# Performance work log

Hardware: AMD Instinct MI355X
Metric: run time of the kernel (lower is better)

## Reference

```python
import jax, jax.numpy as jnp
import numpy as np

T = 256          # n_tokens
APR = 3          # atoms_per_residue
N = T * APR      # n_atoms = 768
CA = 128         # atom_embedding_size
CP = 16          # atom_pair_embedding_size
CT = 384         # token_embedding_size
CS = 384         # single_embedding_size
CZ = 128         # pair_embedding_size
NB = 3           # num_block
H = 4            # num_head
DH = CA // H
NQ = 32          # num_queries (query block size)
NK = 128         # num_keys (local key window)


def _ln(x, g, b):
    m = jnp.mean(x, -1, keepdims=True)
    v = jnp.mean((x - m) ** 2, -1, keepdims=True)
    return (x - m) * jax.lax.rsqrt(v + 1e-5) * g + b


def setup_inputs() -> dict:
    key = jax.random.key(0)
    ks = jax.random.split(key, 32)
    w = lambda k, shape: jax.random.normal(k, shape, jnp.float32) * 0.02
    return {
        "ref_pos": jax.random.normal(ks[0], (N, 3), jnp.float32),
        "ref_space_uid": jax.random.randint(ks[1], (N,), 0, T),
        "r": jax.random.normal(ks[2], (N, 3), jnp.float32),
        "s": jax.random.normal(ks[3], (T, CS), jnp.float32),
        "z": jax.random.normal(ks[4], (T, T, CZ), jnp.float32),
        "W_pos": w(ks[5], (3, CA)),
        "W_pos_offset": w(ks[6], (3, CP)),
        "W_inv_sq_dist": w(ks[7], (1, CP)),
        "W_mask": w(ks[8], (1, CP)),
        "W_cond_a": w(ks[9], (CA, CP)),
        "W_cond_b": w(ks[10], (CA, CP)),
        "ln_s_g": jnp.ones((CS,), jnp.float32), "ln_s_b": jnp.zeros((CS,), jnp.float32),
        "W_single": w(ks[11], (CS, CA)),
        "ln_z_g": jnp.ones((CZ,), jnp.float32), "ln_z_b": jnp.zeros((CZ,), jnp.float32),
        "W_pair": w(ks[12], (CZ, CP)),
        "W_noisy": w(ks[13], (3, CA)),
        "W_mlp1": w(ks[14], (CP, CP)),
        "W_mlp2": w(ks[15], (CP, CP)),
        "W_mlp3": w(ks[16], (CP, CP)),
        "at_ln_g": jnp.ones((NB, CA), jnp.float32), "at_ln_b": jnp.zeros((NB, CA), jnp.float32),
        "at_Wq": w(ks[17], (NB, CA, CA)),
        "at_Wk": w(ks[18], (NB, CA, CA)),
        "at_Wv": w(ks[19], (NB, CA, CA)),
        "at_Wg": w(ks[20], (NB, CA, CA)),
        "at_lnp_g": jnp.ones((NB, CP), jnp.float32), "at_lnp_b": jnp.zeros((NB, CP), jnp.float32),
        "at_Wb": w(ks[21], (NB, CP, H)),
        "at_Wo": w(ks[22], (NB, CA, CA)),
        "at_ln2_g": jnp.ones((NB, CA), jnp.float32), "at_ln2_b": jnp.zeros((NB, CA), jnp.float32),
        "at_Wt1": w(ks[23], (NB, CA, 4 * CA)),
        "at_Wt2": w(ks[24], (NB, 4 * CA, CA)),
        "W_proj": w(ks[25], (CA, CT)),
    }


def _forward(ref_pos, ref_space_uid, r, s, z, W_pos, W_pos_offset, W_inv_sq_dist, W_mask,
             W_cond_a, W_cond_b, ln_s_g, ln_s_b, W_single, ln_z_g, ln_z_b, W_pair, W_noisy,
             W_mlp1, W_mlp2, W_mlp3, at_ln_g, at_ln_b, at_Wq, at_Wk, at_Wv, at_Wg,
             at_lnp_g, at_lnp_b, at_Wb, at_Wo, at_ln2_g, at_ln2_b, at_Wt1, at_Wt2, W_proj):
    c = ref_pos @ W_pos                                             # [N,CA]
    dist = ref_pos[:, None, :] - ref_pos[None, :, :]                # [N,N,3]
    maskf = (ref_space_uid[:, None] == ref_space_uid[None, :])[..., None].astype(jnp.float32)
    pair = (dist @ W_pos_offset) * maskf                            # [N,N,CP]
    sq = jnp.sum(dist * dist, -1, keepdims=True)                    # [N,N,1]
    pair = pair + ((1.0 / (1.0 + sq)) @ W_inv_sq_dist) * maskf
    pair = pair + (maskf @ W_mask) * maskf
    q = c
    # r is not None branch
    c = c + _ln(jnp.tile(s, (APR, 1)), ln_s_g, ln_s_b) @ W_single
    pair = pair + _ln(jnp.tile(z, (APR, APR, 1)), ln_z_g, ln_z_b) @ W_pair
    q = q + r @ W_noisy
    rc = jax.nn.relu(c)
    pair = pair + (rc @ W_cond_a)[:, None, :] + (rc @ W_cond_b)[None, :, :]
    h = jax.nn.relu(pair) @ W_mlp1
    h = jax.nn.relu(h) @ W_mlp2
    h = jax.nn.relu(h) @ W_mlp3
    pair = pair + h
    # sequence-local attention mask (AF3-style: query blocks of NQ attend a NK-wide window)
    idx = jnp.arange(N)
    center = (idx // NQ) * NQ + (NQ - 1) / 2.0
    beta = jnp.where(jnp.abs(idx[None, :].astype(jnp.float32) - center[:, None]) < NK / 2.0, 0.0, -1e9)
    scale = 1.0 / np.sqrt(DH).astype(np.float32)
    x = q
    for b in range(NB):
        a = _ln(x, at_ln_g[b], at_ln_b[b])
        qh = (a @ at_Wq[b]).reshape(N, H, DH)
        kh = (a @ at_Wk[b]).reshape(N, H, DH)
        vh = (a @ at_Wv[b]).reshape(N, H, DH)
        bias = _ln(pair, at_lnp_g[b], at_lnp_b[b]) @ at_Wb[b]       # [N,N,H]
        logits = jnp.einsum('ihd,jhd->hij', qh, kh) * scale + bias.transpose(2, 0, 1) + beta[None]
        attn = jax.nn.softmax(logits, axis=-1)
        o = jnp.einsum('hij,jhd->ihd', attn, vh)
        g = jax.nn.sigmoid(a @ at_Wg[b]).reshape(N, H, DH)
        x = x + (o * g).reshape(N, CA) @ at_Wo[b]
        t = _ln(x, at_ln2_g[b], at_ln2_b[b])
        x = x + jax.nn.relu(t @ at_Wt1[b]) @ at_Wt2[b]
    qout = jax.nn.relu(x @ W_proj)                                  # [N,CT]
    a_out = jnp.mean(qout.reshape(T, APR, CT), axis=-2)             # [T,CT]
    return a_out, qout, c, pair


def reference(ref_pos, ref_space_uid, r, s, z, W_pos, W_pos_offset, W_inv_sq_dist, W_mask,
              W_cond_a, W_cond_b, ln_s_g, ln_s_b, W_single, ln_z_g, ln_z_b, W_pair, W_noisy,
              W_mlp1, W_mlp2, W_mlp3, at_ln_g, at_ln_b, at_Wq, at_Wk, at_Wv, at_Wg,
              at_lnp_g, at_lnp_b, at_Wb, at_Wo, at_ln2_g, at_ln2_b, at_Wt1, at_Wt2, W_proj):
    return _forward(ref_pos, ref_space_uid, r, s, z, W_pos, W_pos_offset, W_inv_sq_dist, W_mask,
                    W_cond_a, W_cond_b, ln_s_g, ln_s_b, W_single, ln_z_g, ln_z_b, W_pair, W_noisy,
                    W_mlp1, W_mlp2, W_mlp3, at_ln_g, at_ln_b, at_Wq, at_Wk, at_Wv, at_Wg,
                    at_lnp_g, at_lnp_b, at_Wb, at_Wo, at_ln2_g, at_ln2_b, at_Wt1, at_Wt2, W_proj)
```

## Files before the change

### kernel.cpp

```cpp
#include <hip/hip_runtime.h>
#include <math.h>


__device__ __forceinline__ float sigmoidf_(float v) { return 1.f / (1.f + __expf(-v)); }

typedef __attribute__((ext_vector_type(4))) short s16x4;
typedef __attribute__((ext_vector_type(8))) short s16x8;
typedef __attribute__((ext_vector_type(4))) float f32x4;

__device__ __forceinline__ unsigned bfpack(float a, float b) {
  return (__float_as_uint(a) >> 16) | (__float_as_uint(b) & 0xFFFF0000u);
}
__device__ __forceinline__ short bf1(float a) { return (short)(__float_as_uint(a) >> 16); }

__global__ __launch_bounds__(128) void k_tokatoms(
    const float* __restrict__ s, const float* __restrict__ g,
    const float* __restrict__ b, const float* __restrict__ W_single,
    const float* __restrict__ ref_pos, const float* __restrict__ r,
    const float* __restrict__ W_pos, const float* __restrict__ W_noisy,
    const float* __restrict__ Wca, const float* __restrict__ Wcb,
    float* __restrict__ c_out, float* __restrict__ x,
    float* __restrict__ ca, float* __restrict__ cb) {
  int tok = blockIdx.x, t = threadIdx.x;
  __shared__ float sln[384];
  __shared__ float ws[48 * 128];
  __shared__ float red[4];
  __shared__ float rc[128];
  float v0 = s[tok * 384 + t], v1 = s[tok * 384 + 128 + t], v2 = s[tok * 384 + 256 + t];
  float ps = v0 + v1 + v2, pq = v0 * v0 + v1 * v1 + v2 * v2;
#pragma unroll
  for (int o = 1; o < 64; o <<= 1) { ps += __shfl_xor(ps, o); pq += __shfl_xor(pq, o); }
  if ((t & 63) == 0) { red[t >> 6] = ps; red[2 + (t >> 6)] = pq; }
  __syncthreads();
  float mean = (red[0] + red[1]) * (1.f / 384.f);
  float var = (red[2] + red[3]) * (1.f / 384.f) - mean * mean;
  float rstd = rsqrtf(var + 1e-5f);
  sln[t] = (v0 - mean) * rstd * g[t] + b[t];
  sln[128 + t] = (v1 - mean) * rstd * g[128 + t] + b[128 + t];
  sln[256 + t] = (v2 - mean) * rstd * g[256 + t] + b[256 + t];
  float ctv = 0.f;
  for (int c0 = 0; c0 < 384; c0 += 48) {
    __syncthreads();
#pragma unroll
    for (int m = 0; m < 12; m++) {
      int idx = (t + 128 * m) * 4;
      *(float4*)&ws[idx] = *(const float4*)&W_single[c0 * 128 + idx];
    }
    __syncthreads();
#pragma unroll 8
    for (int kk = 0; kk < 48; kk++) ctv += sln[c0 + kk] * ws[kk * 128 + t];
  }
  float wp0 = W_pos[t], wp1 = W_pos[128 + t], wp2 = W_pos[256 + t];
  float wn0 = W_noisy[t], wn1 = W_noisy[128 + t], wn2 = W_noisy[256 + t];
#pragma unroll
  for (int a = 0; a < 3; a++) {
    int i = tok + 256 * a;
    float p0 = ref_pos[i * 3], p1 = ref_pos[i * 3 + 1], p2 = ref_pos[i * 3 + 2];
    float r0 = r[i * 3], r1 = r[i * 3 + 1], r2 = r[i * 3 + 2];
    float c0 = p0 * wp0 + p1 * wp1 + p2 * wp2;
    x[i * 128 + t] = c0 + r0 * wn0 + r1 * wn1 + r2 * wn2;
    float cc = c0 + ctv;
    c_out[i * 128 + t] = cc;
    __syncthreads();
    rc[t] = fmaxf(cc, 0.f);
    __syncthreads();
    int out_id = t >> 2, q = t & 3;
    const float* Wm = (out_id < 16) ? Wca : Wcb;
    int ch = out_id & 15;
    float acc = 0.f;
#pragma unroll
    for (int kk = 0; kk < 32; kk++) { int k = q * 32 + kk; acc += rc[k] * Wm[k * 16 + ch]; }
    acc += __shfl_xor(acc, 1);
    acc += __shfl_xor(acc, 2);
    if (q == 0) { if (out_id < 16) ca[i * 16 + ch] = acc; else cb[i * 16 + ch] = acc; }
  }
}

__global__ __launch_bounds__(256) void k_zp(
    const float* __restrict__ z, const float* __restrict__ g,
    const float* __restrict__ lb, const float* __restrict__ W_pair,
    float* __restrict__ zp) {
  __shared__ float wT[16][132];
  __shared__ float zs[16][132];
  __shared__ float sWg[16], Bc[16];
  int t = threadIdx.x;
#pragma unroll
  for (int m = 0; m < 8; m++) {
    int e = t + 256 * m;
    int row = e >> 4, ch = e & 15;
    wT[ch][row] = g[row] * W_pair[e];
  }
  __syncthreads();
  if (t < 32) {
    int ch = t & 15;
    float a = 0.f;
    if (t < 16) {
#pragma unroll 8
      for (int k = 0; k < 128; k++) a += wT[ch][k];
      sWg[ch] = a;
    } else {
#pragma unroll 8
      for (int k = 0; k < 128; k++) a += lb[k] * W_pair[k * 16 + ch];
      Bc[ch] = a;
    }
  }
  int row = t >> 4, kk = (t & 15) * 8;
  long base = ((long)blockIdx.x * 16 + row) * 128 + kk;
  float4 a4 = *(const float4*)&z[base];
  float4 b4 = *(const float4*)&z[base + 4];
  *(float4*)&zs[row][kk] = a4;
  *(float4*)&zs[row][kk + 4] = b4;
  float ps = a4.x + a4.y + a4.z + a4.w + b4.x + b4.y + b4.z + b4.w;
  float pq = a4.x * a4.x + a4.y * a4.y + a4.z * a4.z + a4.w * a4.w +
             b4.x * b4.x + b4.y * b4.y + b4.z * b4.z + b4.w * b4.w;
#pragma unroll
  for (int o = 1; o < 16; o <<= 1) { ps += __shfl_xor(ps, o); pq += __shfl_xor(pq, o); }
  float m = ps * (1.f / 128.f);
  float rstd = rsqrtf(pq * (1.f / 128.f) - m * m + 1e-5f);
  __syncthreads();
  int ch = t & 15;
  float dotv = 0.f;
#pragma unroll 8
  for (int k4 = 0; k4 < 32; k4++) {
    float4 zv = *(float4*)&zs[row][k4 * 4];
    float4 wv = *(float4*)&wT[ch][k4 * 4];
    dotv += zv.x * wv.x + zv.y * wv.y + zv.z * wv.z + zv.w * wv.w;
  }
  zp[((long)blockIdx.x * 16 + row) * 16 + ch] = rstd * (dotv - m * sWg[ch]) + Bc[ch];
}

__global__ __launch_bounds__(256) void k_pairM(
    const float* __restrict__ ref_pos, const int* __restrict__ uid,
    const float* __restrict__ Wpo, const float* __restrict__ Wisd,
    const float* __restrict__ Wmask, const float* __restrict__ W1,
    const float* __restrict__ W2, const float* __restrict__ W3,
    const float* __restrict__ zp, const float* __restrict__ ca,
    const float* __restrict__ cb, const float* __restrict__ lnp_g,
    const float* __restrict__ lnp_b, const float* __restrict__ Wb,
    float* __restrict__ pair_out, float* __restrict__ biasA) {
  int i = blockIdx.x / 3, jb = blockIdx.x % 3, t = threadIdx.x;
  __shared__ float jsx[256], jsy[256], jsz[256];
  __shared__ int jsu[256];
  __shared__ __align__(128) short stg[4][1280];
  __shared__ __align__(16) float pfs[4][1056];
  __shared__ float wgb[192];
  __shared__ float kbs[12];
  int jg = jb * 256 + t;
  jsx[t] = ref_pos[jg * 3];
  jsy[t] = ref_pos[jg * 3 + 1];
  jsz[t] = ref_pos[jg * 3 + 2];
  jsu[t] = uid[jg];
  if (t >= 64) {
    int e = t - 64;
    if (e < 192) {
      int bq = e >> 6, k = (e >> 2) & 15, h = e & 3;
      wgb[e] = lnp_g[bq * 16 + k] * Wb[bq * 64 + k * 4 + h];
    }
  }
  if (t >= 48 && t < 60) {
    int e = t - 48, bq = e >> 2, h = e & 3;
    float a = 0.f;
#pragma unroll
    for (int cc = 0; cc < 16; cc++) a += lnp_b[bq * 16 + cc] * Wb[bq * 64 + cc * 4 + h];
    kbs[e] = a;
  }
  int w = t >> 6, l = t & 63;
  int c = l & 15, gr = l >> 4;
  float pix = ref_pos[i * 3], piy = ref_pos[i * 3 + 1], piz = ref_pos[i * 3 + 2];
  int ui = uid[i];
  float w0c = Wpo[c], w1c = Wpo[16 + c], w2c = Wpo[32 + c];
  float wic = Wisd[c], wmc = Wmask[c], cac = ca[i * 16 + c];
  s16x8 bw0 = {bf1(W1[(4 * gr + 0) * 16 + c]), bf1(W1[(4 * gr + 1) * 16 + c]),
               bf1(W1[(4 * gr + 2) * 16 + c]), bf1(W1[(4 * gr + 3) * 16 + c]),
               (short)0, (short)0, (short)0, (short)0};
  s16x8 bw1 = {bf1(W2[(4 * gr + 0) * 16 + c]), bf1(W2[(4 * gr + 1) * 16 + c]),
               bf1(W2[(4 * gr + 2) * 16 + c]), bf1(W2[(4 * gr + 3) * 16 + c]),
               (short)0, (short)0, (short)0, (short)0};
  s16x8 bw2 = {bf1(W3[(4 * gr + 0) * 16 + c]), bf1(W3[(4 * gr + 1) * 16 + c]),
               bf1(W3[(4 * gr + 2) * 16 + c]), bf1(W3[(4 * gr + 3) * 16 + c]),
               (short)0, (short)0, (short)0, (short)0};
  __syncthreads();
  char* sb = (char*)&stg[w][0];
  unsigned sbase = (unsigned)(uintptr_t)sb;
  f32x4 z4 = {0.f, 0.f, 0.f, 0.f};
#pragma unroll
  for (int g = 0; g < 4; g++) {
    float p0_, p1_, p2_, p3_;
    {
      int jl0 = w * 64 + g * 16 + 4 * gr;
#pragma unroll
      for (int r = 0; r < 4; r++) {
        int jloc = jl0 + r;
        int j = jb * 256 + jloc;
        float d0 = pix - jsx[jloc], d1 = piy - jsy[jloc], d2 = piz - jsz[jloc];
        float mk = (ui == jsu[jloc]) ? 1.f : 0.f;
        float inv = 1.f / (1.f + d0 * d0 + d1 * d1 + d2 * d2);
        float zv = zp[((long)((i & 255) << 8) + jloc) * 16 + c];
        float cbv = cb[j * 16 + c];
        float pv = mk * (d0 * w0c + d1 * w1c + d2 * w2c + inv * wic + wmc) + zv + cbv + cac;
        if (r == 0) p0_ = pv; else if (r == 1) p1_ = pv; else if (r == 2) p2_ = pv; else p3_ = pv;
      }
    }
    char* wp = sb + g * 640 + c * 32 + gr * 8;
    unsigned ra = sbase + (unsigned)(g * 640 + c * 8 + gr * 128);
    *(uint2*)wp = make_uint2(bfpack(fmaxf(p0_, 0.f), fmaxf(p1_, 0.f)),
                             bfpack(fmaxf(p2_, 0.f), fmaxf(p3_, 0.f)));
    s16x4 tr0;
    asm volatile("s_waitcnt lgkmcnt(0)\n\tds_read_b64_tr_b16 %0, %1\n\ts_waitcnt lgkmcnt(0)"
                 : "=v"(tr0) : "v"(ra) : "memory");
    s16x8 a8 = {tr0[0], tr0[1], tr0[2], tr0[3], (short)0, (short)0, (short)0, (short)0};
    f32x4 h1 = __builtin_amdgcn_mfma_f32_16x16x32_bf16(a8, bw0, z4, 0, 0, 0);
    *(uint2*)wp = make_uint2(bfpack(fmaxf(h1[0], 0.f), fmaxf(h1[1], 0.f)),
                             bfpack(fmaxf(h1[2], 0.f), fmaxf(h1[3], 0.f)));
    s16x4 tr1;
    asm volatile("s_waitcnt lgkmcnt(0)\n\tds_read_b64_tr_b16 %0, %1\n\ts_waitcnt lgkmcnt(0)"
                 : "=v"(tr1) : "v"(ra) : "memory");
    s16x8 a8b = {tr1[0], tr1[1], tr1[2], tr1[3], (short)0, (short)0, (short)0, (short)0};
    f32x4 h2 = __builtin_amdgcn_mfma_f32_16x16x32_bf16(a8b, bw1, z4, 0, 0, 0);
    *(uint2*)wp = make_uint2(bfpack(fmaxf(h2[0], 0.f), fmaxf(h2[1], 0.f)),
                             bfpack(fmaxf(h2[2], 0.f), fmaxf(h2[3], 0.f)));
    s16x4 tr2;
    asm volatile("s_waitcnt lgkmcnt(0)\n\tds_read_b64_tr_b16 %0, %1\n\ts_waitcnt lgkmcnt(0)"
                 : "=v"(tr2) : "v"(ra) : "memory");
    s16x8 a8c = {tr2[0], tr2[1], tr2[2], tr2[3], (short)0, (short)0, (short)0, (short)0};
    f32x4 h3 = __builtin_amdgcn_mfma_f32_16x16x32_bf16(a8c, bw2, z4, 0, 0, 0);
    float f0 = p0_ + h3[0], f1 = p1_ + h3[1], f2 = p2_ + h3[2], f3 = p3_ + h3[3];
    {
      int jl0 = w * 64 + g * 16 + 4 * gr;
      long pb = ((long)i * 768 + (long)(jb * 256 + jl0)) * 16 + c;
      pair_out[pb] = f0;
      pair_out[pb + 16] = f1;
      pair_out[pb + 32] = f2;
      pair_out[pb + 48] = f3;
    }
    *(float4*)&pfs[w][g * 264 + c * 16 + 4 * gr] = make_float4(f0, f1, f2, f3);
  }
  asm volatile("s_waitcnt lgkmcnt(0)" ::: "memory");
  int qb = i >> 5;
  int j = jb * 256 + t;
  unsigned jw = (unsigned)(j - (qb * 32 - 48));
  if (jw < 128u) {
    int gt = (t >> 4) & 3, jr = t & 15;
    float v[16];
#pragma unroll
    for (int cc = 0; cc < 16; cc++) v[cc] = pfs[w][gt * 264 + cc * 16 + jr];
    float m = 0.f;
#pragma unroll
    for (int cc = 0; cc < 16; cc++) m += v[cc];
    m *= (1.f / 16.f);
    float vv = 0.f;
#pragma unroll
    for (int cc = 0; cc < 16; cc++) { float d = v[cc] - m; vv += d * d; }
    float rs = rsqrtf(vv * (1.f / 16.f) + 1e-5f);
    float nrm[16];
#pragma unroll
    for (int cc = 0; cc < 16; cc++) nrm[cc] = (v[cc] - m) * rs;
    int qi = i & 31;
#pragma unroll
    for (int bq = 0; bq < 3; bq++) {
      float o0 = kbs[bq * 4 + 0], o1 = kbs[bq * 4 + 1];
      float o2 = kbs[bq * 4 + 2], o3 = kbs[bq * 4 + 3];
#pragma unroll
      for (int k = 0; k < 16; k++) {
        float nv = nrm[k];
        float4 wv = *(float4*)&wgb[bq * 64 + k * 4];
        o0 += nv * wv.x; o1 += nv * wv.y; o2 += nv * wv.z; o3 += nv * wv.w;
      }
      long base = (long)(bq * 96 + qb * 4) * 4096 + (long)qi * 128 + jw;
      biasA[base] = o0;
      biasA[base + 4096] = o1;
      biasA[base + 2 * 4096] = o2;
      biasA[base + 3 * 4096] = o3;
    }
  }
}

__global__ __launch_bounds__(256) void k_qkvg(
    const float* __restrict__ x, const float* __restrict__ lng,
    const float* __restrict__ lnb, const float* __restrict__ Wq,
    const float* __restrict__ Wk, const float* __restrict__ Wv,
    const float* __restrict__ Wg, float* __restrict__ qkvg) {
  __shared__ float As[128][18];
  __shared__ float Ws[128][66];
  int t = threadIdx.x;
  int rb = blockIdx.x >> 3, bn = blockIdx.x & 7;
  int r0 = rb * 16;
  const float* Wm = (bn < 2) ? Wq : (bn < 4) ? Wk : (bn < 6) ? Wv : Wg;
  int c0 = (bn & 1) * 64;
  int ncol0 = (bn >> 1) * 128 + c0;
#pragma unroll
  for (int m = 0; m < 8; m++) {
    int idx = t + 256 * m;
    int row = idx >> 4, c4 = (idx & 15) * 4;
    *(float4*)&Ws[row][c4] = *(const float4*)&Wm[row * 128 + c0 + c4];
  }
  {
    int rr = t >> 4, tt = t & 15;
    int row = r0 + rr;
    float4 x0 = *(const float4*)&x[row * 128 + tt * 8];
    float4 x1 = *(const float4*)&x[row * 128 + tt * 8 + 4];
    float ps = x0.x + x0.y + x0.z + x0.w + x1.x + x1.y + x1.z + x1.w;
    float pq = x0.x * x0.x + x0.y * x0.y + x0.z * x0.z + x0.w * x0.w +
               x1.x * x1.x + x1.y * x1.y + x1.z * x1.z + x1.w * x1.w;
#pragma unroll
    for (int o = 1; o < 16; o <<= 1) { ps += __shfl_xor(ps, o); pq += __shfl_xor(pq, o); }
    float m = ps * (1.f / 128.f);
    float rstd = rsqrtf(pq * (1.f / 128.f) - m * m + 1e-5f);
    float4 g0 = *(const float4*)&lng[tt * 8], g1 = *(const float4*)&lng[tt * 8 + 4];
    float4 b0 = *(const float4*)&lnb[tt * 8], b1 = *(const float4*)&lnb[tt * 8 + 4];
    As[tt * 8 + 0][rr] = (x0.x - m) * rstd * g0.x + b0.x;
    As[tt * 8 + 1][rr] = (x0.y - m) * rstd * g0.y + b0.y;
    As[tt * 8 + 2][rr] = (x0.z - m) * rstd * g0.z + b0.z;
    As[tt * 8 + 3][rr] = (x0.w - m) * rstd * g0.w + b0.w;
    As[tt * 8 + 4][rr] = (x1.x - m) * rstd * g1.x + b1.x;
    As[tt * 8 + 5][rr] = (x1.y - m) * rstd * g1.y + b1.y;
    As[tt * 8 + 6][rr] = (x1.z - m) * rstd * g1.z + b1.z;
    As[tt * 8 + 7][rr] = (x1.w - m) * rstd * g1.w + b1.w;
  }
  __syncthreads();
  int ty = t >> 5, tx = t & 31;
  float a00 = 0, a01 = 0, a10 = 0, a11 = 0;
#pragma unroll 8
  for (int k = 0; k < 128; k++) {
    float2 a2 = *(float2*)&As[k][ty * 2];
    float2 w2 = *(float2*)&Ws[k][tx * 2];
    a00 += a2.x * w2.x; a01 += a2.x * w2.y;
    a10 += a2.y * w2.x; a11 += a2.y * w2.y;
  }
  int row = r0 + ty * 2;
  float2 o0 = {a00, a01}, o1 = {a10, a11};
  *(float2*)&qkvg[row * 512 + ncol0 + tx * 2] = o0;
  *(float2*)&qkvg[(row + 1) * 512 + ncol0 + tx * 2] = o1;
}

__global__ __launch_bounds__(256) void k_attn2(
    const float* __restrict__ qkvg, const float* __restrict__ biasb,
    float* __restrict__ og) {
  int qt = blockIdx.x >> 2, h = blockIdx.x & 3, t = threadIdx.x;
  int i0 = qt * 16;
  int qb32 = qt >> 1;
  int lo = qb32 * 32 - 48;
  int qoff = (qt & 1) * 16;
  __shared__ float qs[16][36];
  __shared__ float ks[128][36];
  __shared__ float vs[128][36];
  __shared__ float L[16][132];
  {
    int e = t * 8;
    int qi = e >> 7, k8 = e & 127;
    const float* bb = &biasb[(long)(qb32 * 4 + h) * 4096 + (long)(qoff + qi) * 128];
#pragma unroll
    for (int m = 0; m < 2; m++) {
      int k4 = k8 + m * 4;
      int j4 = lo + k4;
      float4 bv;
      if (j4 >= 0 && j4 <= 764) bv = *(const float4*)&bb[k4];
      else bv = make_float4(-1e30f, -1e30f, -1e30f, -1e30f);
      *(float4*)&L[qi][k4] = bv;
    }
  }
  if (t < 128) {
    int qi = t >> 3, dq = (t & 7) * 4;
    *(float4*)&qs[qi][dq] = *(const float4*)&qkvg[(i0 + qi) * 512 + h * 32 + dq];
  }
  {
    int kj = t >> 1, dh = (t & 1) * 16;
    int j = lo + kj;
    if (j >= 0 && j < 768) {
      const float4* sk = (const float4*)&qkvg[j * 512 + 128 + h * 32 + dh];
      const float4* sv = (const float4*)&qkvg[j * 512 + 256 + h * 32 + dh];
#pragma unroll
      for (int m = 0; m < 4; m++) {
        *(float4*)&ks[kj][dh + 4 * m] = sk[m];
        *(float4*)&vs[kj][dh + 4 * m] = sv[m];
      }
    } else {
      float4 zz = {0, 0, 0, 0};
#pragma unroll
      for (int m = 0; m < 4; m++) {
        *(float4*)&ks[kj][dh + 4 * m] = zz;
        *(float4*)&vs[kj][dh + 4 * m] = zz;
      }
    }
  }
  __syncthreads();
  const float scale = 0.17677669529663687f;
  {
    int qi = t & 15, kb = t >> 4;
    float4 qr[8];
#pragma unroll
    for (int m = 0; m < 8; m++) qr[m] = *(float4*)&qs[qi][m * 4];
#pragma unroll
    for (int kk = 0; kk < 8; kk++) {
      int kj = kb * 8 + kk;
      float acc = 0.f;
#pragma unroll
      for (int m = 0; m < 8; m++) {
        float4 kv = *(float4*)&ks[kj][m * 4];
        acc += qr[m].x * kv.x + qr[m].y * kv.y + qr[m].z * kv.z + qr[m].w * kv.w;
      }
      L[qi][kj] += acc * scale;
    }
  }
  __syncthreads();
  int qi = t >> 4, sg = t & 15;
  float mx = -1e30f;
#pragma unroll
  for (int k2 = 0; k2 < 8; k2++) mx = fmaxf(mx, L[qi][sg * 8 + k2]);
#pragma unroll
  for (int o = 1; o < 16; o <<= 1) mx = fmaxf(mx, __shfl_xor(mx, o));
  float sum = 0.f;
#pragma unroll
  for (int k2 = 0; k2 < 8; k2++) {
    int kj = sg * 8 + k2;
    float e = __expf(L[qi][kj] - mx);
    L[qi][kj] = e;
    sum += e;
  }
#pragma unroll
  for (int o = 1; o < 16; o <<= 1) sum += __shfl_xor(sum, o);
  float rden = 1.f / sum;
  __syncthreads();
  {
    int d2 = (t & 15) * 2;
    float a0 = 0.f, a1 = 0.f;
#pragma unroll 8
    for (int kj = 0; kj < 128; kj++) {
      float p = L[qi][kj];
      float2 v = *(float2*)&vs[kj][d2];
      a0 += p * v.x; a1 += p * v.y;
    }
    int i = i0 + qi;
    float2 gr = *(const float2*)&qkvg[i * 512 + 384 + h * 32 + d2];
    float2 o2;
    o2.x = a0 * rden * sigmoidf_(gr.x);
    o2.y = a1 * rden * sigmoidf_(gr.y);
    *(float2*)&og[i * 128 + h * 32 + d2] = o2;
  }
}

template <int MODE>
__global__ __launch_bounds__(384) void k_fusedT(
    const float* __restrict__ og, const float* __restrict__ Wo,
    const float* __restrict__ g2, const float* __restrict__ b2,
    const float* __restrict__ Wt1, const float* __restrict__ Wt2,
    float* __restrict__ x,
    const float* __restrict__ lng_n, const float* __restrict__ lnb_n,
    const float* __restrict__ Wq, const float* __restrict__ Wk,
    const float* __restrict__ Wv, const float* __restrict__ Wg,
    float* __restrict__ qkvg, const float* __restrict__ W_proj,
    float* __restrict__ out) {
  int t = threadIdx.x;
  int r0 = blockIdx.x * 3;
  __shared__ float osr[3][128];
  __shared__ float xns[3][128];
  __shared__ float asr[3][128];
  __shared__ float hs[3][512];
  __shared__ float part[4][3][128];
  __shared__ float red[12];
  {
    int rr = t >> 7, c = t & 127;
    osr[rr][c] = og[(r0 + rr) * 128 + c];
    xns[rr][c] = x[(r0 + rr) * 128 + c];
  }
  __syncthreads();
  {
    int c4 = (t & 31) * 4, row = (t >> 5) % 3, q = t / 96;
    int k0 = q * 32;
    float a0 = 0.f, a1 = 0.f, a2 = 0.f, a3 = 0.f;
#pragma unroll 8
    for (int kk = 0; kk < 32; kk++) {
      int k = k0 + kk;
      float4 w = *(const float4*)&Wo[k * 128 + c4];
      float av = osr[row][k];
      a0 += av * w.x; a1 += av * w.y; a2 += av * w.z; a3 += av * w.w;
    }
    *(float4*)&part[q][row][c4] = make_float4(a0, a1, a2, a3);
  }
  __syncthreads();
  {
    int rr = t >> 7, c = t & 127;
    float xv = xns[rr][c] + part[0][rr][c] + part[1][rr][c] + part[2][rr][c] + part[3][rr][c];
    float ps = xv, pq = xv * xv;
#pragma unroll
    for (int o = 1; o < 64; o <<= 1) { ps += __shfl_xor(ps, o); pq += __shfl_xor(pq, o); }
    int wv = t >> 6;
    if ((t & 63) == 0) { red[wv] = ps; red[6 + wv] = pq; }
    __syncthreads();
    float mean = (red[2 * rr] + red[2 * rr + 1]) * (1.f / 128.f);
    float var = (red[6 + 2 * rr] + red[6 + 2 * rr + 1]) * (1.f / 128.f) - mean * mean;
    float rstd = rsqrtf(var + 1e-5f);
    xns[rr][c] = xv;
    asr[rr][c] = (xv - mean) * rstd * g2[c] + b2[c];
  }
  __syncthreads();
  {
    int c4 = (t & 127) * 4, row = t >> 7;
    float a0 = 0.f, a1 = 0.f, a2 = 0.f, a3 = 0.f;
#pragma unroll 8
    for (int k = 0; k < 128; k++) {
      float4 w = *(const float4*)&Wt1[k * 512 + c4];
      float av = asr[row][k];
      a0 += av * w.x; a1 += av * w.y; a2 += av * w.z; a3 += av * w.w;
    }
    *(float4*)&hs[row][c4] = make_float4(fmaxf(a0, 0.f), fmaxf(a1, 0.f),
                                         fmaxf(a2, 0.f), fmaxf(a3, 0.f));
  }
  __syncthreads();
  {
    int c4 = (t & 31) * 4, row = (t >> 5) % 3, q = t / 96;
    int k0 = q * 128;
    float a0 = 0.f, a1 = 0.f, a2 = 0.f, a3 = 0.f;
#pragma unroll 8
    for (int kk = 0; kk < 128; kk++) {
      int k = k0 + kk;
      float4 w = *(const float4*)&Wt2[k * 128 + c4];
      float hv = hs[row][k];
      a0 += hv * w.x; a1 += hv * w.y; a2 += hv * w.z; a3 += hv * w.w;
    }
    *(float4*)&part[q][row][c4] = make_float4(a0, a1, a2, a3);
  }
  __syncthreads();
  {
    int rr = t >> 7, c = t & 127;
    float xf = xns[rr][c] + part[0][rr][c] + part[1][rr][c] +
               part[2][rr][c] + part[3][rr][c];
    x[(r0 + rr) * 128 + c] = xf;
    xns[rr][c] = xf;
  }
  if (MODE == 1) {
    __syncthreads();
    {
      int rr = t >> 7, c = t & 127;
      float xv = xns[rr][c];
      float ps = xv, pq = xv * xv;
#pragma unroll
      for (int o = 1; o < 64; o <<= 1) { ps += __shfl_xor(ps, o); pq += __shfl_xor(pq, o); }
      int wv = t >> 6;
      if ((t & 63) == 0) { red[wv] = ps; red[6 + wv] = pq; }
      __syncthreads();
      float mean = (red[2 * rr] + red[2 * rr + 1]) * (1.f / 128.f);
      float var = (red[6 + 2 * rr] + red[6 + 2 * rr + 1]) * (1.f / 128.f) - mean * mean;
      float rstd = rsqrtf(var + 1e-5f);
      asr[rr][c] = (xv - mean) * rstd * lng_n[c] + lnb_n[c];
    }
    __syncthreads();
    {
      int c4 = (t & 127) * 4, row = t >> 7;
      int mtx = c4 >> 7, lc = c4 & 127;
      const float* Wm = (mtx == 0) ? Wq : (mtx == 1) ? Wk : (mtx == 2) ? Wv : Wg;
      float a0 = 0.f, a1 = 0.f, a2 = 0.f, a3 = 0.f;
#pragma unroll 8
      for (int k = 0; k < 128; k++) {
        float4 w = *(const float4*)&Wm[k * 128 + lc];
        float av = asr[row][k];
        a0 += av * w.x; a1 += av * w.y; a2 += av * w.z; a3 += av * w.w;
      }
      *(float4*)&qkvg[(r0 + row) * 512 + c4] = make_float4(a0, a1, a2, a3);
    }
  }
  if (MODE == 2) {
    __syncthreads();
    int tk = blockIdx.x;
    float a0 = 0.f, a1 = 0.f, a2 = 0.f;
#pragma unroll 8
    for (int k = 0; k < 128; k++) {
      float w = W_proj[k * 384 + t];
      a0 += xns[0][k] * w; a1 += xns[1][k] * w; a2 += xns[2][k] * w;
    }
    a0 = fmaxf(a0, 0.f); a1 = fmaxf(a1, 0.f); a2 = fmaxf(a2, 0.f);
    out[98304 + (tk * 3 + 0) * 384 + t] = a0;
    out[98304 + (tk * 3 + 1) * 384 + t] = a1;
    out[98304 + (tk * 3 + 2) * 384 + t] = a2;
    out[tk * 384 + t] = (a0 + a1 + a2) * (1.f / 3.f);
  }
}

extern "C" void kernel_launch(void* const* d_in, const int* in_sizes, int n_in,
                              void* d_out, int out_size, void* d_ws, size_t ws_size,
                              hipStream_t stream) {
  const float* ref_pos  = (const float*)d_in[0];
  const int*   uid      = (const int*)d_in[1];
  const float* r        = (const float*)d_in[2];
  const float* s        = (const float*)d_in[3];
  const float* z        = (const float*)d_in[4];
  const float* W_pos    = (const float*)d_in[5];
  const float* Wpo      = (const float*)d_in[6];
  const float* Wisd     = (const float*)d_in[7];
  const float* Wmask    = (const float*)d_in[8];
  const float* Wca      = (const float*)d_in[9];
  const float* Wcb      = (const float*)d_in[10];
  const float* ln_s_g   = (const float*)d_in[11];
  const float* ln_s_b   = (const float*)d_in[12];
  const float* W_single = (const float*)d_in[13];
  const float* ln_z_g   = (const float*)d_in[14];
  const float* ln_z_b   = (const float*)d_in[15];
  const float* W_pair   = (const float*)d_in[16];
  const float* W_noisy  = (const float*)d_in[17];
  const float* W_mlp1   = (const float*)d_in[18];
  const float* W_mlp2   = (const float*)d_in[19];
  const float* W_mlp3   = (const float*)d_in[20];
  const float* at_ln_g  = (const float*)d_in[21];
  const float* at_ln_b  = (const float*)d_in[22];
  const float* at_Wq    = (const float*)d_in[23];
  const float* at_Wk    = (const float*)d_in[24];
  const float* at_Wv    = (const float*)d_in[25];
  const float* at_Wg    = (const float*)d_in[26];
  const float* at_lnp_g = (const float*)d_in[27];
  const float* at_lnp_b = (const float*)d_in[28];
  const float* at_Wb    = (const float*)d_in[29];
  const float* at_Wo    = (const float*)d_in[30];
  const float* at_ln2_g = (const float*)d_in[31];
  const float* at_ln2_b = (const float*)d_in[32];
  const float* at_Wt1   = (const float*)d_in[33];
  const float* at_Wt2   = (const float*)d_in[34];
  const float* W_proj   = (const float*)d_in[35];
  float* out = (float*)d_out;
  float* W = (float*)d_ws;
  float* x     = W;
  float* ca    = W + 98304;
  float* cb    = W + 110592;
  float* zp    = W + 122880;
  float* biasA = W + 1171456;
  float* qkvg  = W + 2351104;
  float* og    = W + 2744320;

  k_zp<<<4096, 256, 0, stream>>>(z, ln_z_g, ln_z_b, W_pair, zp);
  k_tokatoms<<<256, 128, 0, stream>>>(s, ln_s_g, ln_s_b, W_single, ref_pos, r,
                                      W_pos, W_noisy, Wca, Wcb,
                                      out + 393216, x, ca, cb);
  k_pairM<<<2304, 256, 0, stream>>>(ref_pos, uid, Wpo, Wisd, Wmask, W_mlp1, W_mlp2,
                                    W_mlp3, zp, ca, cb, at_lnp_g, at_lnp_b, at_Wb,
                                    out + 491520, biasA);
  k_qkvg<<<384, 256, 0, stream>>>(x, at_ln_g, at_ln_b, at_Wq, at_Wk, at_Wv, at_Wg, qkvg);
  k_attn2<<<192, 256, 0, stream>>>(qkvg, biasA, og);
  k_fusedT<1><<<256, 384, 0, stream>>>(og, at_Wo, at_ln2_g, at_ln2_b, at_Wt1, at_Wt2, x,
                                       at_ln_g + 128, at_ln_b + 128,
                                       at_Wq + 16384, at_Wk + 16384,
                                       at_Wv + 16384, at_Wg + 16384, qkvg,
                                       nullptr, nullptr);
  k_attn2<<<192, 256, 0, stream>>>(qkvg, biasA + 393216, og);
  k_fusedT<1><<<256, 384, 0, stream>>>(og, at_Wo + 16384, at_ln2_g + 128, at_ln2_b + 128,
                                       at_Wt1 + 65536, at_Wt2 + 65536, x,
                                       at_ln_g + 256, at_ln_b + 256,
                                       at_Wq + 32768, at_Wk + 32768,
                                       at_Wv + 32768, at_Wg + 32768, qkvg,
                                       nullptr, nullptr);
  k_attn2<<<192, 256, 0, stream>>>(qkvg, biasA + 786432, og);
  k_fusedT<2><<<256, 384, 0, stream>>>(og, at_Wo + 32768, at_ln2_g + 256, at_ln2_b + 256,
                                       at_Wt1 + 131072, at_Wt2 + 131072, x,
                                       nullptr, nullptr, nullptr, nullptr,
                                       nullptr, nullptr, nullptr, W_proj, out);
}
```

Measured before the change: 158.4 us.

## Merge independent front-end kernels into shared launches to cut launch count

```diff
diff --git a/kernel.cpp b/kernel.cpp
--- a/kernel.cpp
+++ b/kernel.cpp
@@ -13,7 +13,10 @@
 }
 __device__ __forceinline__ short bf1(float a) { return (short)(__float_as_uint(a) >> 16); }
 
-__global__ __launch_bounds__(128) void k_tokatoms(
+__global__ __launch_bounds__(256) void k_front(
+    const float* __restrict__ z, const float* __restrict__ zg,
+    const float* __restrict__ zlb, const float* __restrict__ W_pair,
+    float* __restrict__ zp,
     const float* __restrict__ s, const float* __restrict__ g,
     const float* __restrict__ b, const float* __restrict__ W_single,
     const float* __restrict__ ref_pos, const float* __restrict__ r,
@@ -21,115 +24,130 @@
     const float* __restrict__ Wca, const float* __restrict__ Wcb,
     float* __restrict__ c_out, float* __restrict__ x,
     float* __restrict__ ca, float* __restrict__ cb) {
-  int tok = blockIdx.x, t = threadIdx.x;
-  __shared__ float sln[384];
-  __shared__ float ws[48 * 128];
-  __shared__ float red[4];
-  __shared__ float rc[128];
-  float v0 = s[tok * 384 + t], v1 = s[tok * 384 + 128 + t], v2 = s[tok * 384 + 256 + t];
-  float ps = v0 + v1 + v2, pq = v0 * v0 + v1 * v1 + v2 * v2;
-#pragma unroll
-  for (int o = 1; o < 64; o <<= 1) { ps += __shfl_xor(ps, o); pq += __shfl_xor(pq, o); }
-  if ((t & 63) == 0) { red[t >> 6] = ps; red[2 + (t >> 6)] = pq; }
-  __syncthreads();
-  float mean = (red[0] + red[1]) * (1.f / 384.f);
-  float var = (red[2] + red[3]) * (1.f / 384.f) - mean * mean;
-  float rstd = rsqrtf(var + 1e-5f);
-  sln[t] = (v0 - mean) * rstd * g[t] + b[t];
-  sln[128 + t] = (v1 - mean) * rstd * g[128 + t] + b[128 + t];
-  sln[256 + t] = (v2 - mean) * rstd * g[256 + t] + b[256 + t];
-  float ctv = 0.f;
-  for (int c0 = 0; c0 < 384; c0 += 48) {
-    __syncthreads();
-#pragma unroll
-    for (int m = 0; m < 12; m++) {
-      int idx = (t + 128 * m) * 4;
-      *(float4*)&ws[idx] = *(const float4*)&W_single[c0 * 128 + idx];
-    }
-    __syncthreads();
-#pragma unroll 8
-    for (int kk = 0; kk < 48; kk++) ctv += sln[c0 + kk] * ws[kk * 128 + t];
-  }
-  float wp0 = W_pos[t], wp1 = W_pos[128 + t], wp2 = W_pos[256 + t];
-  float wn0 = W_noisy[t], wn1 = W_noisy[128 + t], wn2 = W_noisy[256 + t];
-#pragma unroll
-  for (int a = 0; a < 3; a++) {
-    int i = tok + 256 * a;
-    float p0 = ref_pos[i * 3], p1 = ref_pos[i * 3 + 1], p2 = ref_pos[i * 3 + 2];
-    float r0 = r[i * 3], r1 = r[i * 3 + 1], r2 = r[i * 3 + 2];
-    float c0 = p0 * wp0 + p1 * wp1 + p2 * wp2;
-    x[i * 128 + t] = c0 + r0 * wn0 + r1 * wn1 + r2 * wn2;
-    float cc = c0 + ctv;
-    c_out[i * 128 + t] = cc;
-    __syncthreads();
-    rc[t] = fmaxf(cc, 0.f);
-    __syncthreads();
-    int out_id = t >> 2, q = t & 3;
-    const float* Wm = (out_id < 16) ? Wca : Wcb;
-    int ch = out_id & 15;
-    float acc = 0.f;
-#pragma unroll
-    for (int kk = 0; kk < 32; kk++) { int k = q * 32 + kk; acc += rc[k] * Wm[k * 16 + ch]; }
-    acc += __shfl_xor(acc, 1);
-    acc += __shfl_xor(acc, 2);
-    if (q == 0) { if (out_id < 16) ca[i * 16 + ch] = acc; else cb[i * 16 + ch] = acc; }
+  __shared__ __align__(16) float sm[4624];
+  int t = threadIdx.x;
+  int bid = blockIdx.x;
+  if (bid < 4096) {
+    float* wT = sm;
+    float* zs = sm + 2112;
+    float* sWg = sm + 4224;
+    float* Bc = sm + 4240;
+#pragma unroll
+    for (int m = 0; m < 8; m++) {
+      int e = t + 256 * m;
+      int row = e >> 4, ch = e & 15;
+      wT[ch * 132 + row] = zg[row] * W_pair[e];
+    }
+    __syncthreads();
+    if (t < 32) {
+      int ch = t & 15;
+      float a = 0.f;
+      if (t < 16) {
+#pragma unroll 8
+        for (int k = 0; k < 128; k++) a += wT[ch * 132 + k];
+        sWg[ch] = a;
+      } else {
+#pragma unroll 8
+        for (int k = 0; k < 128; k++) a += zlb[k] * W_pair[k * 16 + ch];
+        Bc[ch] = a;
+      }
+    }
+    int row = t >> 4, kk = (t & 15) * 8;
+    long base = ((long)bid * 16 + row) * 128 + kk;
+    float4 a4 = *(const float4*)&z[base];
+    float4 b4 = *(const float4*)&z[base + 4];
+    *(float4*)&zs[row * 132 + kk] = a4;
+    *(float4*)&zs[row * 132 + kk + 4] = b4;
+    float ps = a4.x + a4.y + a4.z + a4.w + b4.x + b4.y + b4.z + b4.w;
+    float pq = a4.x * a4.x + a4.y * a4.y + a4.z * a4.z + a4.w * a4.w +
+               b4.x * b4.x + b4.y * b4.y + b4.z * b4.z + b4.w * b4.w;
+#pragma unroll
+    for (int o = 1; o < 16; o <<= 1) { ps += __shfl_xor(ps, o); pq += __shfl_xor(pq, o); }
+    float m = ps * (1.f / 128.f);
+    float rstd = rsqrtf(pq * (1.f / 128.f) - m * m + 1e-5f);
+    __syncthreads();
+    int ch = t & 15;
+    float dotv = 0.f;
+#pragma unroll 8
+    for (int k4 = 0; k4 < 32; k4++) {
+      float4 zv = *(float4*)&zs[row * 132 + k4 * 4];
+      float4 wv = *(float4*)&wT[ch * 132 + k4 * 4];
+      dotv += zv.x * wv.x + zv.y * wv.y + zv.z * wv.z + zv.w * wv.w;
+    }
+    zp[((long)bid * 16 + row) * 16 + ch] = rstd * (dotv - m * sWg[ch]) + Bc[ch];
+  } else {
+    int tok = bid - 4096;
+    float* sln = sm;
+    float* ws = sm + 384;
+    float* red = sm + 4480;
+    float* rc = sm + 4488;
+    float v0 = 0.f, v1 = 0.f, v2 = 0.f;
+    if (t < 128) {
+      v0 = s[tok * 384 + t]; v1 = s[tok * 384 + 128 + t]; v2 = s[tok * 384 + 256 + t];
+      float ps = v0 + v1 + v2, pq = v0 * v0 + v1 * v1 + v2 * v2;
+#pragma unroll
+      for (int o = 1; o < 64; o <<= 1) { ps += __shfl_xor(ps, o); pq += __shfl_xor(pq, o); }
+      if ((t & 63) == 0) { red[t >> 6] = ps; red[2 + (t >> 6)] = pq; }
+    }
+    __syncthreads();
+    float ctv = 0.f;
+    if (t < 128) {
+      float mean = (red[0] + red[1]) * (1.f / 384.f);
+      float var = (red[2] + red[3]) * (1.f / 384.f) - mean * mean;
+      float rstd = rsqrtf(var + 1e-5f);
+      sln[t] = (v0 - mean) * rstd * g[t] + b[t];
+      sln[128 + t] = (v1 - mean) * rstd * g[128 + t] + b[128 + t];
+      sln[256 + t] = (v2 - mean) * rstd * g[256 + t] + b[256 + t];
+    }
+    for (int c0 = 0; c0 < 384; c0 += 32) {
+      __syncthreads();
+#pragma unroll
+      for (int m = 0; m < 4; m++) {
+        int idx = (t + 256 * m) * 4;
+        *(float4*)&ws[idx] = *(const float4*)&W_single[c0 * 128 + idx];
+      }
+      __syncthreads();
+      if (t < 128) {
+#pragma unroll 8
+        for (int kk = 0; kk < 32; kk++) ctv += sln[c0 + kk] * ws[kk * 128 + t];
+      }
+    }
+    float wp0 = 0.f, wp1 = 0.f, wp2 = 0.f, wn0 = 0.f, wn1 = 0.f, wn2 = 0.f;
+    if (t < 128) {
+      wp0 = W_pos[t]; wp1 = W_pos[128 + t]; wp2 = W_pos[256 + t];
+      wn0 = W_noisy[t]; wn1 = W_noisy[128 + t]; wn2 = W_noisy[256 + t];
+    }
+#pragma unroll
+    for (int a = 0; a < 3; a++) {
+      int i = tok + 256 * a;
+      float cc = 0.f;
+      if (t < 128) {
+        float p0 = ref_pos[i * 3], p1 = ref_pos[i * 3 + 1], p2 = ref_pos[i * 3 + 2];
+        float r0 = r[i * 3], r1 = r[i * 3 + 1], r2 = r[i * 3 + 2];
+        float c0 = p0 * wp0 + p1 * wp1 + p2 * wp2;
+        x[i * 128 + t] = c0 + r0 * wn0 + r1 * wn1 + r2 * wn2;
+        cc = c0 + ctv;
+        c_out[i * 128 + t] = cc;
+      }
+      __syncthreads();
+      if (t < 128) rc[t] = fmaxf(cc, 0.f);
+      __syncthreads();
+      if (t < 128) {
+        int out_id = t >> 2, q = t & 3;
+        const float* Wm = (out_id < 16) ? Wca : Wcb;
+        int ch = out_id & 15;
+        float acc = 0.f;
+#pragma unroll
+        for (int kk = 0; kk < 32; kk++) { int k = q * 32 + kk; acc += rc[k] * Wm[k * 16 + ch]; }
+        acc += __shfl_xor(acc, 1);
+        acc += __shfl_xor(acc, 2);
+        if (q == 0) { if (out_id < 16) ca[i * 16 + ch] = acc; else cb[i * 16 + ch] = acc; }
+      }
+    }
   }
 }
 
-__global__ __launch_bounds__(256) void k_zp(
-    const float* __restrict__ z, const float* __restrict__ g,
-    const float* __restrict__ lb, const float* __restrict__ W_pair,
-    float* __restrict__ zp) {
-  __shared__ float wT[16][132];
-  __shared__ float zs[16][132];
-  __shared__ float sWg[16], Bc[16];
-  int t = threadIdx.x;
-#pragma unroll
-  for (int m = 0; m < 8; m++) {
-    int e = t + 256 * m;
-    int row = e >> 4, ch = e & 15;
-    wT[ch][row] = g[row] * W_pair[e];
-  }
-  __syncthreads();
-  if (t < 32) {
-    int ch = t & 15;
-    float a = 0.f;
-    if (t < 16) {
-#pragma unroll 8
-      for (int k = 0; k < 128; k++) a += wT[ch][k];
-      sWg[ch] = a;
-    } else {
-#pragma unroll 8
-      for (int k = 0; k < 128; k++) a += lb[k] * W_pair[k * 16 + ch];
-      Bc[ch] = a;
-    }
-  }
-  int row = t >> 4, kk = (t & 15) * 8;
-  long base = ((long)blockIdx.x * 16 + row) * 128 + kk;
-  float4 a4 = *(const float4*)&z[base];
-  float4 b4 = *(const float4*)&z[base + 4];
-  *(float4*)&zs[row][kk] = a4;
-  *(float4*)&zs[row][kk + 4] = b4;
-  float ps = a4.x + a4.y + a4.z + a4.w + b4.x + b4.y + b4.z + b4.w;
-  float pq = a4.x * a4.x + a4.y * a4.y + a4.z * a4.z + a4.w * a4.w +
-             b4.x * b4.x + b4.y * b4.y + b4.z * b4.z + b4.w * b4.w;
-#pragma unroll
-  for (int o = 1; o < 16; o <<= 1) { ps += __shfl_xor(ps, o); pq += __shfl_xor(pq, o); }
-  float m = ps * (1.f / 128.f);
-  float rstd = rsqrtf(pq * (1.f / 128.f) - m * m + 1e-5f);
-  __syncthreads();
-  int ch = t & 15;
-  float dotv = 0.f;
-#pragma unroll 8
-  for (int k4 = 0; k4 < 32; k4++) {
-    float4 zv = *(float4*)&zs[row][k4 * 4];
-    float4 wv = *(float4*)&wT[ch][k4 * 4];
-    dotv += zv.x * wv.x + zv.y * wv.y + zv.z * wv.z + zv.w * wv.w;
-  }
-  zp[((long)blockIdx.x * 16 + row) * 16 + ch] = rstd * (dotv - m * sWg[ch]) + Bc[ch];
-}
-
-__global__ __launch_bounds__(256) void k_pairM(
+__global__ __launch_bounds__(256) void k_pairq(
     const float* __restrict__ ref_pos, const int* __restrict__ uid,
     const float* __restrict__ Wpo, const float* __restrict__ Wisd,
     const float* __restrict__ Wmask, const float* __restrict__ W1,
@@ -137,14 +155,54 @@
     const float* __restrict__ zp, const float* __restrict__ ca,
     const float* __restrict__ cb, const float* __restrict__ lnp_g,
     const float* __restrict__ lnp_b, const float* __restrict__ Wb,
-    float* __restrict__ pair_out, float* __restrict__ biasA) {
-  int i = blockIdx.x / 3, jb = blockIdx.x % 3, t = threadIdx.x;
+    float* __restrict__ pair_out, float* __restrict__ biasA,
+    const float* __restrict__ x, const float* __restrict__ lng,
+    const float* __restrict__ lnb, const float* __restrict__ Wq,
+    const float* __restrict__ Wk, const float* __restrict__ Wv,
+    const float* __restrict__ Wg, float* __restrict__ qkvg) {
   __shared__ float jsx[256], jsy[256], jsz[256];
   __shared__ int jsu[256];
   __shared__ __align__(128) short stg[4][1280];
   __shared__ __align__(16) float pfs[4][1056];
   __shared__ float wgb[192];
   __shared__ float kbs[12];
+  int t = threadIdx.x;
+  int bid = blockIdx.x;
+  if (bid >= 2304) {
+    int r0 = (bid - 2304) * 2;
+    float* asr_ = jsx;
+    float* red_ = jsy;
+    int row = t >> 7, c = t & 127;
+    float xv = x[(r0 + row) * 128 + c];
+    {
+      float ps = xv, pq = xv * xv;
+#pragma unroll
+      for (int o = 1; o < 64; o <<= 1) { ps += __shfl_xor(ps, o); pq += __shfl_xor(pq, o); }
+      int wv = t >> 6;
+      if ((t & 63) == 0) { red_[wv] = ps; red_[4 + wv] = pq; }
+      __syncthreads();
+      float mean = (red_[2 * row] + red_[2 * row + 1]) * (1.f / 128.f);
+      float var = (red_[4 + 2 * row] + red_[4 + 2 * row + 1]) * (1.f / 128.f) - mean * mean;
+      float rstd = rsqrtf(var + 1e-5f);
+      asr_[row * 128 + c] = (xv - mean) * rstd * lng[c] + lnb[c];
+    }
+    __syncthreads();
+    {
+      int c4 = (t & 127) * 4, row2 = t >> 7;
+      int mtx = c4 >> 7, lc = c4 & 127;
+      const float* Wm = (mtx == 0) ? Wq : (mtx == 1) ? Wk : (mtx == 2) ? Wv : Wg;
+      float a0 = 0.f, a1 = 0.f, a2 = 0.f, a3 = 0.f;
+#pragma unroll 8
+      for (int k = 0; k < 128; k++) {
+        float4 w = *(const float4*)&Wm[k * 128 + lc];
+        float av = asr_[row2 * 128 + k];
+        a0 += av * w.x; a1 += av * w.y; a2 += av * w.z; a3 += av * w.w;
+      }
+      *(float4*)&qkvg[(r0 + row2) * 512 + c4] = make_float4(a0, a1, a2, a3);
+    }
+    return;
+  }
+  int i = bid / 3, jb = bid % 3;
   int jg = jb * 256 + t;
   jsx[t] = ref_pos[jg * 3];
   jsy[t] = ref_pos[jg * 3 + 1];
@@ -273,64 +331,6 @@
       biasA[base + 3 * 4096] = o3;
     }
   }
-}
-
-__global__ __launch_bounds__(256) void k_qkvg(
-    const float* __restrict__ x, const float* __restrict__ lng,
-    const float* __restrict__ lnb, const float* __restrict__ Wq,
-    const float* __restrict__ Wk, const float* __restrict__ Wv,
-    const float* __restrict__ Wg, float* __restrict__ qkvg) {
-  __shared__ float As[128][18];
-  __shared__ float Ws[128][66];
-  int t = threadIdx.x;
-  int rb = blockIdx.x >> 3, bn = blockIdx.x & 7;
-  int r0 = rb * 16;
-  const float* Wm = (bn < 2) ? Wq : (bn < 4) ? Wk : (bn < 6) ? Wv : Wg;
-  int c0 = (bn & 1) * 64;
-  int ncol0 = (bn >> 1) * 128 + c0;
-#pragma unroll
-  for (int m = 0; m < 8; m++) {
-    int idx = t + 256 * m;
-    int row = idx >> 4, c4 = (idx & 15) * 4;
-    *(float4*)&Ws[row][c4] = *(const float4*)&Wm[row * 128 + c0 + c4];
-  }
-  {
-    int rr = t >> 4, tt = t & 15;
-    int row = r0 + rr;
-    float4 x0 = *(const float4*)&x[row * 128 + tt * 8];
-    float4 x1 = *(const float4*)&x[row * 128 + tt * 8 + 4];
-    float ps = x0.x + x0.y + x0.z + x0.w + x1.x + x1.y + x1.z + x1.w;
-    float pq = x0.x * x0.x + x0.y * x0.y + x0.z * x0.z + x0.w * x0.w +
-               x1.x * x1.x + x1.y * x1.y + x1.z * x1.z + x1.w * x1.w;
-#pragma unroll
-    for (int o = 1; o < 16; o <<= 1) { ps += __shfl_xor(ps, o); pq += __shfl_xor(pq, o); }
-    float m = ps * (1.f / 128.f);
-    float rstd = rsqrtf(pq * (1.f / 128.f) - m * m + 1e-5f);
-    float4 g0 = *(const float4*)&lng[tt * 8], g1 = *(const float4*)&lng[tt * 8 + 4];
-    float4 b0 = *(const float4*)&lnb[tt * 8], b1 = *(const float4*)&lnb[tt * 8 + 4];
-    As[tt * 8 + 0][rr] = (x0.x - m) * rstd * g0.x + b0.x;
-    As[tt * 8 + 1][rr] = (x0.y - m) * rstd * g0.y + b0.y;
-    As[tt * 8 + 2][rr] = (x0.z - m) * rstd * g0.z + b0.z;
-    As[tt * 8 + 3][rr] = (x0.w - m) * rstd * g0.w + b0.w;
-    As[tt * 8 + 4][rr] = (x1.x - m) * rstd * g1.x + b1.x;
-    As[tt * 8 + 5][rr] = (x1.y - m) * rstd * g1.y + b1.y;
-    As[tt * 8 + 6][rr] = (x1.z - m) * rstd * g1.z + b1.z;
-    As[tt * 8 + 7][rr] = (x1.w - m) * rstd * g1.w + b1.w;
-  }
-  __syncthreads();
-  int ty = t >> 5, tx = t & 31;
-  float a00 = 0, a01 = 0, a10 = 0, a11 = 0;
-#pragma unroll 8
-  for (int k = 0; k < 128; k++) {
-    float2 a2 = *(float2*)&As[k][ty * 2];
-    float2 w2 = *(float2*)&Ws[k][tx * 2];
-    a00 += a2.x * w2.x; a01 += a2.x * w2.y;
-    a10 += a2.y * w2.x; a11 += a2.y * w2.y;
-  }
-  int row = r0 + ty * 2;
-  float2 o0 = {a00, a01}, o1 = {a10, a11};
-  *(float2*)&qkvg[row * 512 + ncol0 + tx * 2] = o0;
-  *(float2*)&qkvg[(row + 1) * 512 + ncol0 + tx * 2] = o1;
 }
 
 __global__ __launch_bounds__(256) void k_attn2(
@@ -625,14 +625,15 @@
   float* qkvg  = W + 2351104;
   float* og    = W + 2744320;
 
-  k_zp<<<4096, 256, 0, stream>>>(z, ln_z_g, ln_z_b, W_pair, zp);
-  k_tokatoms<<<256, 128, 0, stream>>>(s, ln_s_g, ln_s_b, W_single, ref_pos, r,
-                                      W_pos, W_noisy, Wca, Wcb,
-                                      out + 393216, x, ca, cb);
-  k_pairM<<<2304, 256, 0, stream>>>(ref_pos, uid, Wpo, Wisd, Wmask, W_mlp1, W_mlp2,
+  k_front<<<4352, 256, 0, stream>>>(z, ln_z_g, ln_z_b, W_pair, zp,
+                                    s, ln_s_g, ln_s_b, W_single, ref_pos, r,
+                                    W_pos, W_noisy, Wca, Wcb,
+                                    out + 393216, x, ca, cb);
+  k_pairq<<<2688, 256, 0, stream>>>(ref_pos, uid, Wpo, Wisd, Wmask, W_mlp1, W_mlp2,
                                     W_mlp3, zp, ca, cb, at_lnp_g, at_lnp_b, at_Wb,
-                                    out + 491520, biasA);
-  k_qkvg<<<384, 256, 0, stream>>>(x, at_ln_g, at_ln_b, at_Wq, at_Wk, at_Wv, at_Wg, qkvg);
+                                    out + 491520, biasA,
+                                    x, at_ln_g, at_ln_b, at_Wq, at_Wk, at_Wv, at_Wg,
+                                    qkvg);
   k_attn2<<<192, 256, 0, stream>>>(qkvg, biasA, og);
   k_fusedT<1><<<256, 384, 0, stream>>>(og, at_Wo, at_ln2_g, at_ln2_b, at_Wt1, at_Wt2, x,
                                        at_ln_g + 128, at_ln_b + 128,
```

Result: no change. 155.9 us (-1.6%).
